# Kernel tuning notes

Hardware: AMD Instinct MI355X
Metric: run time of the kernel (lower is better)

## Reference

```python
import jax, jax.numpy as jnp
import numpy as np

N = 30000
E = 480000
F = 256
H = 32
HEADS = 4
NUM_LABEL = 6
NEG_SLOPE = 0.2
BN_EPS = 1e-5
NUM_ITER = 3
ROUTE_NODES = 2 * (HEADS + HEADS)  # 16
PC_OUT = 8


def squash(t, axis=-1):
    sq = (t ** 2).sum(axis=axis, keepdims=True)
    return (sq / (1.0 + sq)) * t / jnp.sqrt(sq)


def glorot(key, shape):
    fan_in, fan_out = shape[-2], shape[-1]
    s = jnp.sqrt(6.0 / (fan_in + fan_out))
    return jax.random.uniform(key, shape, jnp.float32, -s, s)


def setup_inputs() -> dict:
    key = jax.random.key(0)
    ks = jax.random.split(key, 10)
    x = jax.random.normal(ks[0], (N, F), jnp.float32)
    rng = np.random.default_rng(0)
    src = rng.integers(0, N, E)
    dst = rng.integers(0, N, E)
    dst = np.where(src == dst, (dst + 1) % N, dst)  # no self loops (torch code removes them)
    edge_index = jnp.asarray(np.stack([src, dst]), jnp.int32)
    y = jax.random.randint(ks[1], (N,), 0, NUM_LABEL, jnp.int32)
    return {
        'x': x,
        'gamma': jnp.ones((F,), jnp.float32),
        'beta': jnp.zeros((F,), jnp.float32),
        'W_lin': glorot(ks[2], (F, HEADS * H)),
        'b_lin': jnp.zeros((HEADS * H,), jnp.float32),
        'W_gat': glorot(ks[3], (F, HEADS * H)),
        'att': glorot(ks[4], (1, HEADS, 2 * H)),
        'b_gat': jnp.zeros((HEADS * H,), jnp.float32),
        'Wp': glorot(ks[5], (2, H, PC_OUT)),
        'bp': jnp.zeros((2, PC_OUT), jnp.float32),
        'route_w': jax.random.normal(ks[6], (NUM_LABEL, ROUTE_NODES, PC_OUT, H), jnp.float32),
        'edge_index': edge_index,
        'y': y,
    }


def _forward(x, gamma, beta, W_lin, b_lin, W_gat, att, b_gat, Wp, bp, route_w, edge_index, y):
    n = x.shape[0]
    # BatchNorm1d (training-mode batch statistics, biased variance)
    mean = x.mean(axis=0)
    var = ((x - mean) ** 2).mean(axis=0)
    xb = (x - mean) / jnp.sqrt(var + BN_EPS) * gamma + beta

    hidden = (xb @ W_lin + b_lin).reshape(n, HEADS, H)

    # ---- GATConv (concat=True, add self-loops) ----
    xt = (xb @ W_gat).reshape(n, HEADS, H)
    loop = jnp.arange(n, dtype=edge_index.dtype)
    src = jnp.concatenate([edge_index[0], loop])
    dst = jnp.concatenate([edge_index[1], loop])
    x_i = xt[dst]  # [Et, HEADS, H] target
    x_j = xt[src]  # [Et, HEADS, H] source
    a_i, a_j = att[:, :, :H], att[:, :, H:]
    alpha = (x_i * a_i).sum(-1) + (x_j * a_j).sum(-1)  # [Et, HEADS]
    alpha = jnp.where(alpha >= 0, alpha, NEG_SLOPE * alpha)
    amax = jax.ops.segment_max(alpha, dst, num_segments=n)
    e = jnp.exp(alpha - amax[dst])
    denom = jax.ops.segment_sum(e, dst, num_segments=n)
    alpha = e / (denom[dst] + 1e-16)
    msg = x_j * alpha[:, :, None]
    aggr = jax.ops.segment_sum(msg, dst, num_segments=n)  # [n, HEADS, H]
    gat_out = aggr.reshape(n, HEADS * H) + b_gat

    xc = jnp.concatenate([gat_out.reshape(n, HEADS, H), hidden], axis=1)  # [n, 2*HEADS, H]
    xc = jax.nn.relu(xc)

    # ---- primary capsules: 2 Linear(H->8), cat on route axis, squash ----
    pc = jnp.einsum('nrh,cho->ncro', xc, Wp) + bp[None, :, None, :]  # [n,2,8,8]
    u = squash(pc.reshape(n, ROUTE_NODES, PC_OUT))  # [n,16,8]

    # ---- digit capsules: dynamic routing (softmax over route nodes, dim=2) ----
    priors = jnp.einsum('nri,crio->cnro', u, route_w)  # [6,n,16,H]
    logits = jnp.zeros(priors.shape[:3], priors.dtype)  # [6,n,16]
    for it in range(NUM_ITER):
        probs = jax.nn.softmax(logits, axis=2)
        v = squash((probs[..., None] * priors).sum(axis=2))  # [6,n,H]
        if it != NUM_ITER - 1:
            logits = logits + (priors * v[:, :, None, :]).sum(-1)

    xo = v.transpose(1, 0, 2)  # [n,6,H]
    features = xo.reshape(n, NUM_LABEL * H)
    output = jnp.sqrt((xo ** 2).sum(-1))  # [n,6] capsule lengths
    logp = jax.nn.log_softmax(output, axis=-1)
    loss = -jnp.take_along_axis(logp, y[:, None].astype(jnp.int32), axis=1).mean()
    return output, loss, features


def reference(x, gamma, beta, W_lin, b_lin, W_gat, att, b_gat, Wp, bp, route_w, edge_index, y):
    return _forward(x, gamma, beta, W_lin, b_lin, W_gat, att, b_gat, Wp, bp, route_w, edge_index, y)
```

## Files before the change

### kernel.cpp

```cpp
#include <hip/hip_runtime.h>
#include <hip/hip_bf16.h>

#define NND 30000
#define NE  480000
#define FD  256
#define HD  32
#define HEADS 4
#define NLAB 6
#define NEG_SLOPE 0.2f
#define BN_EPS 1e-5f
#define LOG2E 1.44269504f

#define WS_FLAG      0
#define WS_BNSUM     4
#define WS_BNSQ      260
#define WS_LOSS      516
#define WS_COUNTS    520
#define WS_ZERO_ELEMS 30524
#define WS_OFFSETS   30524
#define WS_CURSOR    60528
#define WS_GAMMA     90528
#define WS_BETA      90784
#define WS_WLIN      91040
#define WS_BLIN      123808
#define WS_WGAT      123936
#define WS_ATT       156704
#define WS_BGAT      156960
#define WS_WP        157088
#define WS_BP        157600
#define WS_RW        157616
#define WS_SCALE     182192
#define WS_SHIFT     182448
#define WS_WC        182704
#define WS_BC        248240
#define WS_SD        248496
#define WS_SS        368496
#define WS_ONORM     488496
#define WS_CSR       668496
#define WS_XF        1178496
#define WS_U         1178496
#define WS_BLKSUM    5018496
#define WS_BLKOFF    5018624
#define WS_Y         8858496
#define WS_XCG       16538496

#define OUT_LOSS_IDX 180000
#define OUT_FEAT_IDX 180001

#define SCAN_NB 118

__device__ __forceinline__ float lrelu(float a) { return a >= 0.0f ? a : NEG_SLOPE * a; }

#if __has_builtin(__builtin_amdgcn_rcpf)
__device__ __forceinline__ float frcp(float x) { return __builtin_amdgcn_rcpf(x); }
#else
__device__ __forceinline__ float frcp(float x) { return 1.0f / x; }
#endif
#if __has_builtin(__builtin_amdgcn_sqrtf)
__device__ __forceinline__ float fsqrt(float x) { return __builtin_amdgcn_sqrtf(x); }
#else
__device__ __forceinline__ float fsqrt(float x) { return sqrtf(x); }
#endif
#if __has_builtin(__builtin_amdgcn_exp2f)
__device__ __forceinline__ float fexp2(float x) { return __builtin_amdgcn_exp2f(x); }
#else
__device__ __forceinline__ float fexp2(float x) { return exp2f(x); }
#endif

__device__ __forceinline__ void pin(float& x) { asm volatile("" : "+v"(x)); }

template<int CTRL>
__device__ __forceinline__ float fdpp(float v) {
    return __int_as_float(__builtin_amdgcn_mov_dpp(__float_as_int(v), CTRL, 0xF, 0xF, true));
}
template<int PAT>
__device__ __forceinline__ float fswz(float v) {
    return __int_as_float(__builtin_amdgcn_ds_swizzle(__float_as_int(v), PAT));
}
__device__ __forceinline__ float redq(float v) {
    v += fdpp<0xB1>(v);
    v += fdpp<0x4E>(v);
    v += fswz<0x101F>(v);
    v += fswz<0x201F>(v);
    v += fswz<0x401F>(v);
    return v;
}
__device__ __forceinline__ float redq_sum64(float v) {
    v = redq(v);
    return v + __shfl_xor(v, 32);
}
__device__ __forceinline__ float redq_max64(float v) {
    v = fmaxf(v, fdpp<0xB1>(v));
    v = fmaxf(v, fdpp<0x4E>(v));
    v = fmaxf(v, fswz<0x101F>(v));
    v = fmaxf(v, fswz<0x201F>(v));
    v = fmaxf(v, fswz<0x401F>(v));
    return fmaxf(v, __shfl_xor(v, 32));
}
__device__ __forceinline__ void dreduce(float dp[8], int k, float out[8]) {
    #pragma unroll
    for (int j = 0; j < 8; ++j) {
        dp[j] += fdpp<0xB1>(dp[j]);
        dp[j] += fdpp<0x4E>(dp[j]);
    }
    float A = (k == 0) ? dp[0] : (k == 1) ? dp[1] : (k == 2) ? dp[2] : dp[3];
    float B = (k == 0) ? dp[4] : (k == 1) ? dp[5] : (k == 2) ? dp[6] : dp[7];
    A += fswz<0x101F>(A); A += fswz<0x201F>(A); A += fswz<0x401F>(A);
    B += fswz<0x101F>(B); B += fswz<0x201F>(B); B += fswz<0x401F>(B);
    out[0] = fdpp<0x00>(A); out[1] = fdpp<0x55>(A); out[2] = fdpp<0xAA>(A); out[3] = fdpp<0xFF>(A);
    out[4] = fdpp<0x00>(B); out[5] = fdpp<0x55>(B); out[6] = fdpp<0xAA>(B); out[7] = fdpp<0xFF>(B);
}

__global__ void k_detect(const unsigned int* gamma_raw, int* flag) {
    unsigned int w = gamma_raw[0];
    *flag = ((w & 0xFFFFu) == 0x3F80u) ? 1 : 0;
}

__device__ __forceinline__ float cvt_load(const void* p, int i, int f) {
    if (f) return __bfloat162float(((const __hip_bfloat16*)p)[i]);
    return ((const float*)p)[i];
}

__global__ void k_convert(const void* src, float* dst, int n, const int* flagp) {
    int f = *flagp;
    for (int i = blockIdx.x * blockDim.x + threadIdx.x; i < n; i += gridDim.x * blockDim.x)
        dst[i] = cvt_load(src, i, f);
}

__global__ void k_convert_params(const void* p0, const void* p1, const void* p2, const void* p3,
                                 const void* p4, const void* p5, const void* p6, const void* p7,
                                 const void* p8, const void* p9, float* dst, const int* flagp) {
    int f = *flagp;
    int i = blockIdx.x * blockDim.x + threadIdx.x;
    if (i >= 91664) return;
    const void* p; int off;
    if      (i < 256)   { p = p0; off = i; }
    else if (i < 512)   { p = p1; off = i - 256; }
    else if (i < 33280) { p = p2; off = i - 512; }
    else if (i < 33408) { p = p3; off = i - 33280; }
    else if (i < 66176) { p = p4; off = i - 33408; }
    else if (i < 66432) { p = p5; off = i - 66176; }
    else if (i < 66560) { p = p6; off = i - 66432; }
    else if (i < 67072) { p = p7; off = i - 66560; }
    else if (i < 67088) { p = p8; off = i - 67072; }
    else                { p = p9; off = i - 67088; }
    dst[i] = cvt_load(p, off, f);
}

__global__ void k_bn_stats(const float* xf, float* bn_sum, float* bn_sq) {
    int t = threadIdx.x;
    int rows = (NND + gridDim.x - 1) / gridDim.x;
    int r0 = blockIdx.x * rows;
    int r1 = min(NND, r0 + rows);
    float s = 0.0f, ss = 0.0f;
    for (int r = r0; r < r1; ++r) {
        float v = xf[(size_t)r * FD + t];
        s += v; ss += v * v;
    }
    atomicAdd(&bn_sum[t], s);
    atomicAdd(&bn_sq[t], ss);
}

__global__ void k_bn_final(const float* bn_sum, const float* bn_sq, const float* gamma,
                           const float* beta, float* scale, float* shift) {
    int t = threadIdx.x;
    float mean = bn_sum[t] / (float)NND;
    float var  = bn_sq[t] / (float)NND - mean * mean;
    float inv  = 1.0f / sqrtf(var + BN_EPS);
    float sc   = gamma[t] * inv;
    scale[t] = sc;
    shift[t] = beta[t] - mean * sc;
}

__global__ void k_fold(const float* wlin, const float* wgat, const float* blin,
                       const float* scale, const float* shift, float* Wc, float* bc) {
    int j = blockIdx.x;
    int k = threadIdx.x;
    float w = (j < 128) ? wlin[k * 128 + j] : wgat[k * 128 + (j - 128)];
    Wc[k * 256 + j] = scale[k] * w;
    __shared__ float red[256];
    red[k] = shift[k] * w;
    __syncthreads();
    for (int s = 128; s > 0; s >>= 1) { if (k < s) red[k] += red[k + s]; __syncthreads(); }
    if (k == 0) bc[j] = red[0] + (j < 128 ? blin[j] : 0.0f);
}

__global__ __launch_bounds__(256) void k_gemm(const float* A, const float* B,
                                              const float* bias, float* C) {
    __shared__ __align__(16) float As[16][128];
    __shared__ __align__(16) float Bs[16][64];
    int t  = threadIdx.x;
    int bm = blockIdx.x * 128;
    int bn = blockIdx.y * 64;
    int tr = t / 16, tc = t % 16;
    float acc[8][4] = {};
    int alm = t >> 2;
    int alk = (t & 3) * 4;
    int blk = t >> 4;
    int bln = (t & 15) * 4;
    for (int k0 = 0; k0 < 256; k0 += 16) {
        #pragma unroll
        for (int half = 0; half < 2; ++half) {
            int row = bm + alm + half * 64;
            float4 av = make_float4(0.f, 0.f, 0.f, 0.f);
            if (row < NND) av = *(const float4*)(A + (size_t)row * 256 + k0 + alk);
            int m = alm + half * 64;
            As[alk + 0][m] = av.x; As[alk + 1][m] = av.y;
            As[alk + 2][m] = av.z; As[alk + 3][m] = av.w;
        }
        float4 bv = *(const float4*)(B + (size_t)(k0 + blk) * 256 + bn + bln);
        *(float4*)&Bs[blk][bln] = bv;
        __syncthreads();
        #pragma unroll
        for (int kk = 0; kk < 16; ++kk) {
            float a[8], b[4];
            *(float4*)&a[0] = *(const float4*)&As[kk][tr * 8];
            *(float4*)&a[4] = *(const float4*)&As[kk][tr * 8 + 4];
            *(float4*)&b[0] = *(const float4*)&Bs[kk][tc * 4];
            #pragma unroll
            for (int i = 0; i < 8; ++i)
                #pragma unroll
                for (int j = 0; j < 4; ++j) acc[i][j] += a[i] * b[j];
        }
        __syncthreads();
    }
    #pragma unroll
    for (int i = 0; i < 8; ++i) {
        int row = bm + tr * 8 + i;
        if (row < NND) {
            int col = bn + tc * 4;
            float4 o;
            o.x = acc[i][0] + bias[col + 0];
            o.y = acc[i][1] + bias[col + 1];
            o.z = acc[i][2] + bias[col + 2];
            o.w = acc[i][3] + bias[col + 3];
            *(float4*)(C + (size_t)row * 256 + col) = o;
        }
    }
}

__global__ void k_scores(const float* Y, const float* attf, float* sD, float* sS) {
    int idx = blockIdx.x * blockDim.x + threadIdx.x;
    if (idx >= NND * HEADS) return;
    int n = idx >> 2, h = idx & 3;
    const float* xrow = Y + (size_t)n * 256 + 128 + h * 32;
    const float* ai = attf + h * 64;
    const float* aj = ai + 32;
    float si = 0.f, sj = 0.f;
    #pragma unroll
    for (int k = 0; k < 32; ++k) { float v = xrow[k]; si += v * ai[k]; sj += v * aj[k]; }
    sD[idx] = si * LOG2E; sS[idx] = sj * LOG2E;
}

__global__ void k_count(const int* ei, int* counts) {
    int e = blockIdx.x * blockDim.x + threadIdx.x;
    if (e >= NE + NND) return;
    int d = (e < NE) ? ei[NE + e] : (e - NE);
    atomicAdd(&counts[d], 1);
}

__global__ void k_scan_blk(const int* counts, int* offsets, int* blksum) {
    int t = threadIdx.x, b = blockIdx.x;
    int i = b * 256 + t;
    int v = (i < NND) ? counts[i] : 0;
    int lane = t & 63, wv = t >> 6;
    int x = v;
    #pragma unroll
    for (int off = 1; off < 64; off <<= 1) {
        int y = __shfl_up(x, off);
        if (lane >= off) x += y;
    }
    __shared__ int wsum[4];
    if (lane == 63) wsum[wv] = x;
    __syncthreads();
    int add = 0;
    #pragma unroll
    for (int w = 0; w < 4; ++w) add += (w < wv) ? wsum[w] : 0;
    if (i < NND) offsets[i] = add + x - v;
    if (t == 255) blksum[b] = add + x;
}

__global__ void k_scan_top(const int* blksum, int* blkoff) {
    int t = threadIdx.x;
    int v = (t < SCAN_NB) ? blksum[t] : 0;
    int lane = t & 63, wv = t >> 6;
    int x = v;
    #pragma unroll
    for (int off = 1; off < 64; off <<= 1) {
        int y = __shfl_up(x, off);
        if (lane >= off) x += y;
    }
    __shared__ int ws2[2];
    if (lane == 63) ws2[wv] = x;
    __syncthreads();
    int add = (wv == 1) ? ws2[0] : 0;
    if (t < SCAN_NB) blkoff[t] = add + x - v;
}

__global__ void k_scan_add(const int* blkoff, int* offsets, int* cursor) {
    int i = blockIdx.x * 256 + threadIdx.x;
    if (i >= NND) return;
    int o = offsets[i] + blkoff[blockIdx.x];
    offsets[i] = o;
    cursor[i] = o;
}

__global__ void k_scatter(const int* ei, int* cursor, int* csr) {
    int e = blockIdx.x * blockDim.x + threadIdx.x;
    if (e >= NE + NND) return;
    int s, d;
    if (e < NE) { s = ei[e]; d = ei[NE + e]; } else { s = d = e - NE; }
    int pos = atomicAdd(&cursor[d], 1);
    csr[pos] = s;
}

__global__ __launch_bounds__(256) void k_aggr(const float* Y, const float* sD, const float* sS,
                                              const int* offsets, const int* counts, const int* csr,
                                              const float* bgat, float* xcg) {
    int wave = (blockIdx.x * blockDim.x + threadIdx.x) >> 6;
    int lane = threadIdx.x & 63;
    if (wave >= NND) return;
    int n = wave;
    int start = offsets[n], deg = counts[n];
    float4 sd = *(const float4*)(sD + (size_t)n * 4);
    float m0 = -1e30f, m1 = -1e30f, m2 = -1e30f, m3 = -1e30f;
    for (int e = lane; e < deg; e += 64) {
        int s = csr[start + e];
        float4 sj = *(const float4*)(sS + (size_t)s * 4);
        m0 = fmaxf(m0, lrelu(sd.x + sj.x));
        m1 = fmaxf(m1, lrelu(sd.y + sj.y));
        m2 = fmaxf(m2, lrelu(sd.z + sj.z));
        m3 = fmaxf(m3, lrelu(sd.w + sj.w));
    }
    m0 = redq_max64(m0); m1 = redq_max64(m1);
    m2 = redq_max64(m2); m3 = redq_max64(m3);
    float s0 = 0.f, s1 = 0.f, s2 = 0.f, s3 = 0.f;
    for (int e = lane; e < deg; e += 64) {
        int s = csr[start + e];
        float4 sj = *(const float4*)(sS + (size_t)s * 4);
        s0 += fexp2(lrelu(sd.x + sj.x) - m0);
        s1 += fexp2(lrelu(sd.y + sj.y) - m1);
        s2 += fexp2(lrelu(sd.z + sj.z) - m2);
        s3 += fexp2(lrelu(sd.w + sj.w) - m3);
    }
    s0 = redq_sum64(s0); s1 = redq_sum64(s1);
    s2 = redq_sum64(s2); s3 = redq_sum64(s3);
    float i0 = frcp(s0 + 1e-16f), i1 = frcp(s1 + 1e-16f);
    float i2 = frcp(s2 + 1e-16f), i3 = frcp(s3 + 1e-16f);
    float acc0 = 0.f, acc1 = 0.f;
    int hA = lane >> 5;
    for (int base = 0; base < deg; base += 64) {
        int cnt = min(64, deg - base);
        int sidx = 0; float w0 = 0.f, w1 = 0.f, w2 = 0.f, w3 = 0.f;
        if (base + lane < deg) {
            sidx = csr[start + base + lane];
            float4 sj = *(const float4*)(sS + (size_t)sidx * 4);
            w0 = fexp2(lrelu(sd.x + sj.x) - m0) * i0;
            w1 = fexp2(lrelu(sd.y + sj.y) - m1) * i1;
            w2 = fexp2(lrelu(sd.z + sj.z) - m2) * i2;
            w3 = fexp2(lrelu(sd.w + sj.w) - m3) * i3;
        }
        for (int j = 0; j < cnt; ++j) {
            int s2i = __builtin_amdgcn_readlane(sidx, j);
            float wa0 = __int_as_float(__builtin_amdgcn_readlane(__float_as_int(w0), j));
            float wa1 = __int_as_float(__builtin_amdgcn_readlane(__float_as_int(w1), j));
            float wb0 = __int_as_float(__builtin_amdgcn_readlane(__float_as_int(w2), j));
            float wb1 = __int_as_float(__builtin_amdgcn_readlane(__float_as_int(w3), j));
            float wA = hA ? wa1 : wa0;
            float wB = hA ? wb1 : wb0;
            const float* xrow = Y + (size_t)s2i * 256 + 128;
            acc0 += wA * xrow[lane];
            acc1 += wB * xrow[64 + lane];
        }
    }
    float r0 = acc0 + bgat[lane];
    float r1 = acc1 + bgat[64 + lane];
    xcg[(size_t)n * 128 + lane]      = r0 > 0.f ? r0 : 0.f;
    xcg[(size_t)n * 128 + 64 + lane] = r1 > 0.f ? r1 : 0.f;
}

__global__ __launch_bounds__(256, 4) void k_u(const float* Y, const float* xcg,
                                              const float* Wpf, const float* bpf, float* uG) {
    int lane = threadIdx.x & 63;
    int gw = blockIdx.x * 4 + (threadIdx.x >> 6);
    int nwaves = gridDim.x * 4;
    int r = lane >> 3, oo = lane & 7;
    float wpA[32], wpB[32];
    #pragma unroll
    for (int k = 0; k < 32; ++k) {
        wpA[k] = Wpf[k * 8 + oo];
        wpB[k] = Wpf[256 + k * 8 + oo];
    }
    #pragma unroll
    for (int k = 0; k < 32; ++k) { pin(wpA[k]); pin(wpB[k]); }
    float bpA = bpf[oo], bpB = bpf[8 + oo];
    for (int n = gw; n < NND; n += nwaves) {
        const float* rowp = (r < 4) ? (xcg + (size_t)n * 128 + r * 32)
                                    : (Y + (size_t)n * 256 + (r - 4) * 32);
        float pcA = bpA, pcB = bpB;
        #pragma unroll
        for (int k4 = 0; k4 < 8; ++k4) {
            float4 xv = *(const float4*)(rowp + k4 * 4);
            xv.x = fmaxf(xv.x, 0.f); xv.y = fmaxf(xv.y, 0.f);
            xv.z = fmaxf(xv.z, 0.f); xv.w = fmaxf(xv.w, 0.f);
            pcA += xv.x * wpA[k4*4+0] + xv.y * wpA[k4*4+1] + xv.z * wpA[k4*4+2] + xv.w * wpA[k4*4+3];
            pcB += xv.x * wpB[k4*4+0] + xv.y * wpB[k4*4+1] + xv.z * wpB[k4*4+2] + xv.w * wpB[k4*4+3];
        }
        float sA = pcA * pcA, sB = pcB * pcB;
        sA += fdpp<0xB1>(sA); sA += fdpp<0x4E>(sA); sA += fswz<0x101F>(sA);
        sB += fdpp<0xB1>(sB); sB += fdpp<0x4E>(sB); sB += fswz<0x101F>(sB);
        float cA = fsqrt(sA) * frcp(1.0f + sA);
        float cB = fsqrt(sB) * frcp(1.0f + sB);
        uG[(size_t)n * 128 + lane]      = pcA * cA;
        uG[(size_t)n * 128 + 64 + lane] = pcB * cB;
    }
}

__global__ __launch_bounds__(256, 3) void k_route3(const float* uG, const float* rwf,
                                                   float* onorm, void* dout, const int* flagp) {
    int flag = *flagp;
    int t = threadIdx.x;
    int lane = t & 63;
    int c = blockIdx.x % 6;
    int wv = t >> 6;
    int widx = (blockIdx.x / 6) * 4 + wv;
    int nstep = (gridDim.x / 6) * 4;
    int h = lane >> 5, o = lane & 31;
    int k = lane & 3;
    float rw[8][8];
    #pragma unroll
    for (int j = 0; j < 8; ++j)
        #pragma unroll
        for (int i = 0; i < 8; ++i)
            rw[j][i] = rwf[(((c * 16) + (h * 8 + j)) * 8 + i) * 32 + o];
    #pragma unroll
    for (int j = 0; j < 8; ++j)
        #pragma unroll
        for (int i = 0; i < 8; ++i)
            pin(rw[j][i]);
    float* outf = (float*)dout;
    __hip_bfloat16* outb = (__hip_bfloat16*)dout;
    for (int n = widx; n < NND; n += nstep) {
        const float* up = uG + (size_t)n * 128 + h * 64;
        float p[8];
        #pragma unroll
        for (int j = 0; j < 8; ++j) {
            float4 a = *(const float4*)(up + j * 8);
            float4 b = *(const float4*)(up + j * 8 + 4);
            p[j] = a.x*rw[j][0] + a.y*rw[j][1] + a.z*rw[j][2] + a.w*rw[j][3]
                 + b.x*rw[j][4] + b.y*rw[j][5] + b.z*rw[j][6] + b.w*rw[j][7];
        }
        float tl = p[0]+p[1]+p[2]+p[3]+p[4]+p[5]+p[6]+p[7];
        float s = (tl + __shfl_xor(tl, 32)) * 0.0625f;
        float sq = redq(s * s);
        float v = s * (fsqrt(sq) * frcp(1.0f + sq));
        float vs = v * LOG2E;
        float logits[8], dp[8];
        #pragma unroll
        for (int j = 0; j < 8; ++j) dp[j] = p[j] * vs;
        dreduce(dp, k, logits);
        float sq3 = 0.f, v3 = 0.f;
        #pragma unroll
        for (int it = 0; it < 2; ++it) {
            float m01 = fmaxf(logits[0], logits[1]);
            float m23 = fmaxf(logits[2], logits[3]);
            float m45 = fmaxf(logits[4], logits[5]);
            float m67 = fmaxf(logits[6], logits[7]);
            float mx = fmaxf(fmaxf(m01, m23), fmaxf(m45, m67));
            mx = fmaxf(mx, __shfl_xor(mx, 32));
            float e[8]; float se = 0.f;
            #pragma unroll
            for (int j = 0; j < 8; ++j) { e[j] = fexp2(logits[j] - mx); se += e[j]; }
            se += __shfl_xor(se, 32);
            float inv = frcp(se);
            float sl = 0.f;
            #pragma unroll
            for (int j = 0; j < 8; ++j) sl += e[j] * p[j];
            sl *= inv;
            float ss = sl + __shfl_xor(sl, 32);
            float q = redq(ss * ss);
            float vv = ss * (fsqrt(q) * frcp(1.0f + q));
            if (it == 0) {
                float dd[8], lu[8];
                float vvs = vv * LOG2E;
                #pragma unroll
                for (int j = 0; j < 8; ++j) dd[j] = p[j] * vvs;
                dreduce(dd, k, lu);
                #pragma unroll
                for (int j = 0; j < 8; ++j) logits[j] += lu[j];
            } else { v3 = vv; sq3 = q; }
        }
        if (lane < 32) {
            size_t fidx = (size_t)OUT_FEAT_IDX + (size_t)n * 192 + c * 32 + o;
            if (flag) outb[fidx] = __float2bfloat16(v3); else outf[fidx] = v3;
            if (lane == 0) {
                float norm = sq3 * frcp(1.0f + sq3);
                onorm[n * 6 + c] = norm;
                size_t oidx = (size_t)n * 6 + c;
                if (flag) outb[oidx] = __float2bfloat16(norm); else outf[oidx] = norm;
            }
        }
    }
}

__global__ void k_loss(const float* onorm, const int* y, float* acc) {
    float l = 0.f;
    for (int n = blockIdx.x * blockDim.x + threadIdx.x; n < NND; n += gridDim.x * blockDim.x) {
        const float* v = onorm + n * 6;
        float m = v[0];
        #pragma unroll
        for (int cc = 1; cc < 6; ++cc) m = fmaxf(m, v[cc]);
        float s = 0.f;
        #pragma unroll
        for (int cc = 0; cc < 6; ++cc) s += __expf(v[cc] - m);
        l += m + __logf(s) - v[y[n]];
    }
    __shared__ float red[256];
    red[threadIdx.x] = l;
    __syncthreads();
    for (int s = 128; s > 0; s >>= 1) { if (threadIdx.x < s) red[threadIdx.x] += red[threadIdx.x + s]; __syncthreads(); }
    if (threadIdx.x == 0) atomicAdd(acc, red[0]);
}

__global__ void k_loss_fin(const float* acc, void* dout, const int* flagp) {
    float v = acc[0] / (float)NND;
    if (*flagp) ((__hip_bfloat16*)dout)[OUT_LOSS_IDX] = __float2bfloat16(v);
    else        ((float*)dout)[OUT_LOSS_IDX] = v;
}

extern "C" void kernel_launch(void* const* d_in, const int* in_sizes, int n_in,
                              void* d_out, int out_size, void* d_ws, size_t ws_size,
                              hipStream_t stream) {
    (void)in_sizes; (void)n_in; (void)out_size; (void)ws_size;
    float* ws = (float*)d_ws;
    int*  wsi = (int*)d_ws;
    const int* ei = (const int*)d_in[11];
    const int* y  = (const int*)d_in[12];

    hipMemsetAsync(d_ws, 0, (size_t)WS_ZERO_ELEMS * 4, stream);
    k_detect<<<1, 1, 0, stream>>>((const unsigned int*)d_in[1], wsi + WS_FLAG);

    k_convert<<<2048, 256, 0, stream>>>(d_in[0], ws + WS_XF, NND * FD, wsi + WS_FLAG);
    k_convert_params<<<(91664 + 255) / 256, 256, 0, stream>>>(
        d_in[1], d_in[2], d_in[3], d_in[4], d_in[5], d_in[6], d_in[7], d_in[8], d_in[9], d_in[10],
        ws + WS_GAMMA, wsi + WS_FLAG);

    k_bn_stats<<<120, 256, 0, stream>>>(ws + WS_XF, ws + WS_BNSUM, ws + WS_BNSQ);
    k_bn_final<<<1, 256, 0, stream>>>(ws + WS_BNSUM, ws + WS_BNSQ, ws + WS_GAMMA, ws + WS_BETA,
                                      ws + WS_SCALE, ws + WS_SHIFT);
    k_fold<<<256, 256, 0, stream>>>(ws + WS_WLIN, ws + WS_WGAT, ws + WS_BLIN,
                                    ws + WS_SCALE, ws + WS_SHIFT, ws + WS_WC, ws + WS_BC);

    k_gemm<<<dim3((NND + 127) / 128, 4), 256, 0, stream>>>(ws + WS_XF, ws + WS_WC, ws + WS_BC, ws + WS_Y);

    k_scores<<<(NND * HEADS + 255) / 256, 256, 0, stream>>>(ws + WS_Y, ws + WS_ATT, ws + WS_SD, ws + WS_SS);

    k_count<<<(NE + NND + 255) / 256, 256, 0, stream>>>(ei, wsi + WS_COUNTS);
    k_scan_blk<<<SCAN_NB, 256, 0, stream>>>(wsi + WS_COUNTS, wsi + WS_OFFSETS, wsi + WS_BLKSUM);
    k_scan_top<<<1, 128, 0, stream>>>(wsi + WS_BLKSUM, wsi + WS_BLKOFF);
    k_scan_add<<<SCAN_NB, 256, 0, stream>>>(wsi + WS_BLKOFF, wsi + WS_OFFSETS, wsi + WS_CURSOR);
    k_scatter<<<(NE + NND + 255) / 256, 256, 0, stream>>>(ei, wsi + WS_CURSOR, wsi + WS_CSR);

    k_aggr<<<(NND + 3) / 4, 256, 0, stream>>>(ws + WS_Y, ws + WS_SD, ws + WS_SS,
                                              wsi + WS_OFFSETS, wsi + WS_COUNTS, wsi + WS_CSR,
                                              ws + WS_BGAT, ws + WS_XCG);

    k_u<<<512, 256, 0, stream>>>(ws + WS_Y, ws + WS_XCG, ws + WS_WP, ws + WS_BP, ws + WS_U);
    k_route3<<<3072, 256, 0, stream>>>(ws + WS_U, ws + WS_RW, ws + WS_ONORM, d_out, wsi + WS_FLAG);

    k_loss<<<118, 256, 0, stream>>>(ws + WS_ONORM, y, ws + WS_LOSS);
    k_loss_fin<<<1, 1, 0, stream>>>(ws + WS_LOSS, d_out, wsi + WS_FLAG);
}
```

Baseline: 512.6 us.

## Process two nodes per wave in routing and use DPP/permlane reductions

Replaces ds_swizzle and shfl-based cross-lane reductions with DPP row shifts and gfx950 permlane16/32 swap instructions, which avoid LDS-path latency. The routing kernel now handles two nodes per loop iteration so their independent reduction chains can interleave and hide latency. The softmax-weighted sum is fused into the exp loop, and launch bounds drop from 3 to 2 blocks per SIMD to make room for the extra registers. The cost is higher register pressure and lower occupancy.

```diff
diff --git a/kernel.cpp b/kernel.cpp
--- a/kernel.cpp
+++ b/kernel.cpp
@@ -77,25 +77,47 @@
 __device__ __forceinline__ float fswz(float v) {
     return __int_as_float(__builtin_amdgcn_ds_swizzle(__float_as_int(v), PAT));
 }
+
+#if __has_builtin(__builtin_amdgcn_permlane16_swap)
+__device__ __forceinline__ float2 pl16(float v) {
+    unsigned int u = __float_as_uint(v);
+    auto r = __builtin_amdgcn_permlane16_swap(u, u, false, false);
+    return make_float2(__uint_as_float(r[0]), __uint_as_float(r[1]));
+}
+#else
+__device__ __forceinline__ float2 pl16(float v) { return make_float2(v, fswz<0x401F>(v)); }
+#endif
+#if __has_builtin(__builtin_amdgcn_permlane32_swap)
+__device__ __forceinline__ float2 pl32(float v) {
+    unsigned int u = __float_as_uint(v);
+    auto r = __builtin_amdgcn_permlane32_swap(u, u, false, false);
+    return make_float2(__uint_as_float(r[0]), __uint_as_float(r[1]));
+}
+#else
+__device__ __forceinline__ float2 pl32(float v) { return make_float2(v, __shfl_xor(v, 32)); }
+#endif
+
 __device__ __forceinline__ float redq(float v) {
     v += fdpp<0xB1>(v);
     v += fdpp<0x4E>(v);
-    v += fswz<0x101F>(v);
-    v += fswz<0x201F>(v);
-    v += fswz<0x401F>(v);
-    return v;
+    v += fdpp<0x124>(v);
+    v += fdpp<0x128>(v);
+    float2 r = pl16(v);
+    return r.x + r.y;
 }
 __device__ __forceinline__ float redq_sum64(float v) {
     v = redq(v);
-    return v + __shfl_xor(v, 32);
+    float2 r = pl32(v);
+    return r.x + r.y;
 }
 __device__ __forceinline__ float redq_max64(float v) {
     v = fmaxf(v, fdpp<0xB1>(v));
     v = fmaxf(v, fdpp<0x4E>(v));
-    v = fmaxf(v, fswz<0x101F>(v));
-    v = fmaxf(v, fswz<0x201F>(v));
-    v = fmaxf(v, fswz<0x401F>(v));
-    return fmaxf(v, __shfl_xor(v, 32));
+    v = fmaxf(v, fdpp<0x124>(v));
+    v = fmaxf(v, fdpp<0x128>(v));
+    float2 a = pl16(v); v = fmaxf(a.x, a.y);
+    float2 b = pl32(v);
+    return fmaxf(b.x, b.y);
 }
 __device__ __forceinline__ void dreduce(float dp[8], int k, float out[8]) {
     #pragma unroll
@@ -105,8 +127,10 @@
     }
     float A = (k == 0) ? dp[0] : (k == 1) ? dp[1] : (k == 2) ? dp[2] : dp[3];
     float B = (k == 0) ? dp[4] : (k == 1) ? dp[5] : (k == 2) ? dp[6] : dp[7];
-    A += fswz<0x101F>(A); A += fswz<0x201F>(A); A += fswz<0x401F>(A);
-    B += fswz<0x101F>(B); B += fswz<0x201F>(B); B += fswz<0x401F>(B);
+    A += fdpp<0x124>(A); A += fdpp<0x128>(A);
+    B += fdpp<0x124>(B); B += fdpp<0x128>(B);
+    float2 ra = pl16(A); A = ra.x + ra.y;
+    float2 rb = pl16(B); B = rb.x + rb.y;
     out[0] = fdpp<0x00>(A); out[1] = fdpp<0x55>(A); out[2] = fdpp<0xAA>(A); out[3] = fdpp<0xFF>(A);
     out[4] = fdpp<0x00>(B); out[5] = fdpp<0x55>(B); out[6] = fdpp<0xAA>(B); out[7] = fdpp<0xFF>(B);
 }
@@ -407,8 +431,8 @@
             pcB += xv.x * wpB[k4*4+0] + xv.y * wpB[k4*4+1] + xv.z * wpB[k4*4+2] + xv.w * wpB[k4*4+3];
         }
         float sA = pcA * pcA, sB = pcB * pcB;
-        sA += fdpp<0xB1>(sA); sA += fdpp<0x4E>(sA); sA += fswz<0x101F>(sA);
-        sB += fdpp<0xB1>(sB); sB += fdpp<0x4E>(sB); sB += fswz<0x101F>(sB);
+        sA += fdpp<0xB1>(sA); sA += fdpp<0x4E>(sA); sA += fdpp<0x141>(sA);
+        sB += fdpp<0xB1>(sB); sB += fdpp<0x4E>(sB); sB += fdpp<0x141>(sB);
         float cA = fsqrt(sA) * frcp(1.0f + sA);
         float cB = fsqrt(sB) * frcp(1.0f + sB);
         uG[(size_t)n * 128 + lane]      = pcA * cA;
@@ -416,7 +440,7 @@
     }
 }
 
-__global__ __launch_bounds__(256, 3) void k_route3(const float* uG, const float* rwf,
+__global__ __launch_bounds__(256, 2) void k_route3(const float* uG, const float* rwf,
                                                    float* onorm, void* dout, const int* flagp) {
     int flag = *flagp;
     int t = threadIdx.x;
@@ -440,64 +464,98 @@
             pin(rw[j][i]);
     float* outf = (float*)dout;
     __hip_bfloat16* outb = (__hip_bfloat16*)dout;
-    for (int n = widx; n < NND; n += nstep) {
-        const float* up = uG + (size_t)n * 128 + h * 64;
-        float p[8];
+    for (int n0 = widx; n0 < NND; n0 += 2 * nstep) {
+        int n1 = n0 + nstep;
+        int act1 = (n1 < NND);
+        int n1c = act1 ? n1 : n0;
+        const float* up[2];
+        up[0] = uG + (size_t)n0  * 128 + h * 64;
+        up[1] = uG + (size_t)n1c * 128 + h * 64;
+        float p[2][8];
         #pragma unroll
         for (int j = 0; j < 8; ++j) {
-            float4 a = *(const float4*)(up + j * 8);
-            float4 b = *(const float4*)(up + j * 8 + 4);
-            p[j] = a.x*rw[j][0] + a.y*rw[j][1] + a.z*rw[j][2] + a.w*rw[j][3]
-                 + b.x*rw[j][4] + b.y*rw[j][5] + b.z*rw[j][6] + b.w*rw[j][7];
-        }
-        float tl = p[0]+p[1]+p[2]+p[3]+p[4]+p[5]+p[6]+p[7];
-        float s = (tl + __shfl_xor(tl, 32)) * 0.0625f;
-        float sq = redq(s * s);
-        float v = s * (fsqrt(sq) * frcp(1.0f + sq));
-        float vs = v * LOG2E;
-        float logits[8], dp[8];
-        #pragma unroll
-        for (int j = 0; j < 8; ++j) dp[j] = p[j] * vs;
-        dreduce(dp, k, logits);
-        float sq3 = 0.f, v3 = 0.f;
+            #pragma unroll
+            for (int q = 0; q < 2; ++q) {
+                float4 a = *(const float4*)(up[q] + j * 8);
+                float4 b = *(const float4*)(up[q] + j * 8 + 4);
+                p[q][j] = a.x*rw[j][0] + a.y*rw[j][1] + a.z*rw[j][2] + a.w*rw[j][3]
+                        + b.x*rw[j][4] + b.y*rw[j][5] + b.z*rw[j][6] + b.w*rw[j][7];
+            }
+        }
+        float logits[2][8];
+        float vL[2];
+        #pragma unroll
+        for (int q = 0; q < 2; ++q) {
+            float tl = ((p[q][0]+p[q][1])+(p[q][2]+p[q][3]))+((p[q][4]+p[q][5])+(p[q][6]+p[q][7]));
+            float2 r = pl32(tl);
+            float s = (r.x + r.y) * 0.0625f;
+            float sqv = redq(s * s);
+            vL[q] = s * (fsqrt(sqv) * frcp(1.0f + sqv));
+        }
+        #pragma unroll
+        for (int q = 0; q < 2; ++q) {
+            float dp[8];
+            float vs = vL[q] * LOG2E;
+            #pragma unroll
+            for (int j = 0; j < 8; ++j) dp[j] = p[q][j] * vs;
+            dreduce(dp, k, logits[q]);
+        }
+        float sq3[2], v3[2];
         #pragma unroll
         for (int it = 0; it < 2; ++it) {
-            float m01 = fmaxf(logits[0], logits[1]);
-            float m23 = fmaxf(logits[2], logits[3]);
-            float m45 = fmaxf(logits[4], logits[5]);
-            float m67 = fmaxf(logits[6], logits[7]);
-            float mx = fmaxf(fmaxf(m01, m23), fmaxf(m45, m67));
-            mx = fmaxf(mx, __shfl_xor(mx, 32));
-            float e[8]; float se = 0.f;
+            float vv[2], qq[2];
             #pragma unroll
-            for (int j = 0; j < 8; ++j) { e[j] = fexp2(logits[j] - mx); se += e[j]; }
-            se += __shfl_xor(se, 32);
-            float inv = frcp(se);
-            float sl = 0.f;
+            for (int q = 0; q < 2; ++q) {
+                float m01 = fmaxf(logits[q][0], logits[q][1]);
+                float m23 = fmaxf(logits[q][2], logits[q][3]);
+                float m45 = fmaxf(logits[q][4], logits[q][5]);
+                float m67 = fmaxf(logits[q][6], logits[q][7]);
+                float mx = fmaxf(fmaxf(m01, m23), fmaxf(m45, m67));
+                float2 rm = pl32(mx);
+                mx = fmaxf(rm.x, rm.y);
+                float se = 0.f, sl = 0.f;
+                #pragma unroll
+                for (int j = 0; j < 8; ++j) {
+                    float ee = fexp2(logits[q][j] - mx);
+                    se += ee; sl += ee * p[q][j];
+                }
+                float2 rs = pl32(se);
+                float2 rl = pl32(sl);
+                float ss = (rl.x + rl.y) * frcp(rs.x + rs.y);
+                float qv = redq(ss * ss);
+                vv[q] = ss * (fsqrt(qv) * frcp(1.0f + qv));
+                qq[q] = qv;
+            }
+            if (it == 0) {
+                #pragma unroll
+                for (int q = 0; q < 2; ++q) {
+                    float dd[8], lu[8];
+                    float vvs = vv[q] * LOG2E;
+                    #pragma unroll
+                    for (int j = 0; j < 8; ++j) dd[j] = p[q][j] * vvs;
+                    dreduce(dd, k, lu);
+                    #pragma unroll
+                    for (int j = 0; j < 8; ++j) logits[q][j] += lu[j];
+                }
+            } else {
+                #pragma unroll
+                for (int q = 0; q < 2; ++q) { v3[q] = vv[q]; sq3[q] = qq[q]; }
+            }
+        }
+        if (lane < 32) {
             #pragma unroll
-            for (int j = 0; j < 8; ++j) sl += e[j] * p[j];
-            sl *= inv;
-            float ss = sl + __shfl_xor(sl, 32);
-            float q = redq(ss * ss);
-            float vv = ss * (fsqrt(q) * frcp(1.0f + q));
-            if (it == 0) {
-                float dd[8], lu[8];
-                float vvs = vv * LOG2E;
-                #pragma unroll
-                for (int j = 0; j < 8; ++j) dd[j] = p[j] * vvs;
-                dreduce(dd, k, lu);
-                #pragma unroll
-                for (int j = 0; j < 8; ++j) logits[j] += lu[j];
-            } else { v3 = vv; sq3 = q; }
-        }
-        if (lane < 32) {
-            size_t fidx = (size_t)OUT_FEAT_IDX + (size_t)n * 192 + c * 32 + o;
-            if (flag) outb[fidx] = __float2bfloat16(v3); else outf[fidx] = v3;
-            if (lane == 0) {
-                float norm = sq3 * frcp(1.0f + sq3);
-                onorm[n * 6 + c] = norm;
-                size_t oidx = (size_t)n * 6 + c;
-                if (flag) outb[oidx] = __float2bfloat16(norm); else outf[oidx] = norm;
+            for (int q = 0; q < 2; ++q) {
+                if (q == 0 || act1) {
+                    int n = q ? n1 : n0;
+                    size_t fidx = (size_t)OUT_FEAT_IDX + (size_t)n * 192 + c * 32 + o;
+                    if (flag) outb[fidx] = __float2bfloat16(v3[q]); else outf[fidx] = v3[q];
+                    if (lane == 0) {
+                        float norm = sq3[q] * frcp(1.0f + sq3[q]);
+                        onorm[n * 6 + c] = norm;
+                        size_t oidx = (size_t)n * 6 + c;
+                        if (flag) outb[oidx] = __float2bfloat16(norm); else outf[oidx] = norm;
+                    }
+                }
             }
         }
     }
```

Result: slower. 550.6 us (+7.4%).
